# Kernel optimization log

Hardware: AMD Instinct MI355X
Metric: run time of the kernel (lower is better)

Reference implementation:

```python
import jax, jax.numpy as jnp
import numpy as np

INPUT_SIZE = 128
HIDDEN = 256
EPS = 1e-5  # PyTorch BatchNorm1d default


def setup_inputs() -> dict:
    key = jax.random.key(0)
    k1, k2, k3 = jax.random.split(key, 3)
    B, S = 128, 1024
    x = jax.random.normal(k1, (B, S, INPUT_SIZE), dtype=jnp.float32)
    fan_in = INPUT_SIZE + HIDDEN
    bound = 1.0 / np.sqrt(fan_in)
    # Linear(input+hidden -> 4*hidden); stored transposed for x @ W
    W = jax.random.uniform(k2, (fan_in, 4 * HIDDEN), minval=-bound, maxval=bound, dtype=jnp.float32)
    b = jax.random.uniform(k3, (4 * HIDDEN,), minval=-bound, maxval=bound, dtype=jnp.float32)
    gamma = jnp.ones((4, HIDDEN), dtype=jnp.float32)   # per-gate BN weight
    beta = jnp.zeros((4, HIDDEN), dtype=jnp.float32)   # per-gate BN bias
    return {"x": x, "W": W, "b": b, "gamma": gamma, "beta": beta}


def reference(x, W, b, gamma, beta):
    B, S, _ = x.shape
    H = HIDDEN

    def step(carry, x_t):
        hx, cx = carry
        g = jnp.concatenate([x_t, hx], axis=1) @ W + b          # [B, 4H]
        g = g.reshape(B, 4, H)
        # BatchNorm1d (training mode): batch statistics per gate/feature
        mean = g.mean(axis=0)                                   # [4, H]
        var = jnp.mean((g - mean) ** 2, axis=0)                 # biased var
        gn = (g - mean) * jax.lax.rsqrt(var + EPS) * gamma + beta
        i = jax.nn.sigmoid(gn[:, 0])
        f = jax.nn.sigmoid(gn[:, 1])
        c = jnp.tanh(gn[:, 2])
        o = jax.nn.sigmoid(gn[:, 3])
        cy = f * cx + i * c
        hy = o * jnp.tanh(cy)
        return (hy, cy), hy

    h0 = jnp.zeros((B, H), dtype=x.dtype)
    c0 = jnp.zeros((B, H), dtype=x.dtype)
    (hy, cy), outs = jax.lax.scan(step, (h0, c0), jnp.swapaxes(x, 0, 1))
    outputs = jnp.swapaxes(outs, 0, 1)                          # [B, S, H]
    return outputs, hy, cy
```

## Files before the change

kernel.cpp:

```cpp
#include <hip/hip_runtime.h>

#define BATCH 128
#define SEQ   1024
#define INSZ  128
#define HID   256
#define NBLK  32
#define NTHR  512
#define FPB   8
#define EPSV  1e-5f

typedef __attribute__((ext_vector_type(4))) float f32x4;
typedef __attribute__((ext_vector_type(8))) short short8;
typedef __attribute__((ext_vector_type(4))) unsigned u32x4;
typedef unsigned u32;

__device__ __forceinline__ unsigned short f2bf(float f) {
  unsigned u = __builtin_bit_cast(unsigned, f);
  u += 0x7FFFu + ((u >> 16) & 1u);
  return (unsigned short)(u >> 16);
}
__device__ __forceinline__ short8 xcvt(float4 f0, float4 f1) {
  u32 a, b, c, d2;
  asm("v_cvt_pk_bf16_f32 %0, %1, %2" : "=v"(a)  : "v"(f0.x), "v"(f0.y));
  asm("v_cvt_pk_bf16_f32 %0, %1, %2" : "=v"(b)  : "v"(f0.z), "v"(f0.w));
  asm("v_cvt_pk_bf16_f32 %0, %1, %2" : "=v"(c)  : "v"(f1.x), "v"(f1.y));
  asm("v_cvt_pk_bf16_f32 %0, %1, %2" : "=v"(d2) : "v"(f1.z), "v"(f1.w));
  u32x4 t = {a, b, c, d2};
  return __builtin_bit_cast(short8, t);
}

__launch_bounds__(NTHR)
__global__ void bnlstm_kernel(const float* __restrict__ x,
                              const float* __restrict__ W,
                              const float* __restrict__ gamma,
                              const float* __restrict__ beta,
                              float* __restrict__ out,
                              unsigned short* __restrict__ hbuf,
                              u32* __restrict__ flags) {
  __shared__ __attribute__((aligned(16))) unsigned short Zs[32 * 1024];
  __shared__ float red1[2][8][32];
  __shared__ float red2[2][8][32];
  __shared__ float waveTr[8][16][17];
  __shared__ __attribute__((aligned(16))) unsigned short hpack[8][16][8];

  const int tid   = threadIdx.x;
  const int bid   = blockIdx.x;
  const int lane  = tid & 63;
  const int wid   = tid >> 6;
  const int col16 = lane & 15;
  const int kg    = lane >> 4;
  const int d     = col16 & 3;
  const int q     = col16 >> 2;
  const int arow  = wid * 16 + col16;
  const int brow  = wid * 16 + kg * 4 + d;

  short8 wf[2][12];
  for (int cg = 0; cg < 2; ++cg) {
    const int c32 = cg * 16 + col16;
    const int wcol = (c32 & 3) * HID + bid * FPB + (c32 >> 2);
    for (int kt = 0; kt < 12; ++kt) {
      short8 v;
      for (int e = 0; e < 8; ++e)
        v[e] = (short)f2bf(W[(kt * 32 + kg * 8 + e) * 1024 + wcol]);
      wf[cg][kt] = v;
    }
  }
  float gam = 0.f, bet = 0.f;
  if (lane < 32) {
    gam = gamma[(lane & 3) * HID + bid * FPB + (lane >> 2)];
    bet = beta [(lane & 3) * HID + bid * FPB + (lane >> 2)];
  }

  float cst[2] = {0.f, 0.f};
  float hnv[2];

  const float* xbase = x + (size_t)arow * (SEQ * INSZ) + kg * 8;
  float4 xv[8];
  #pragma unroll
  for (int kt = 0; kt < 4; ++kt) {
    xv[2 * kt]     = *(const float4*)(xbase + kt * 32);
    xv[2 * kt + 1] = *(const float4*)(xbase + kt * 32 + 4);
  }

  for (int t = 0; t < SEQ; ++t) {
    const int pR = t & 1;
    f32x4 acc0 = {0.f, 0.f, 0.f, 0.f}, acc1 = {0.f, 0.f, 0.f, 0.f};

    #pragma unroll
    for (int kt = 0; kt < 4; ++kt) {
      short8 ax = xcvt(xv[2 * kt], xv[2 * kt + 1]);
      acc0 = __builtin_amdgcn_mfma_f32_16x16x32_bf16(ax, wf[0][kt], acc0, 0, 0, 0);
      acc1 = __builtin_amdgcn_mfma_f32_16x16x32_bf16(ax, wf[1][kt], acc1, 0, 0, 0);
    }
    if (t + 1 < SEQ) {
      const float* xr = xbase + (size_t)(t + 1) * INSZ;
      #pragma unroll
      for (int kt = 0; kt < 4; ++kt) {
        xv[2 * kt]     = *(const float4*)(xr + kt * 32);
        xv[2 * kt + 1] = *(const float4*)(xr + kt * 32 + 4);
      }
    }

    if (t > 0) {
      {
        const u32 tv = (u32)t;
        while (true) {
          u32 v = (lane < 4)
            ? __hip_atomic_load(&flags[(wid * 4 + lane) * 32], __ATOMIC_RELAXED,
                                __HIP_MEMORY_SCOPE_AGENT)
            : tv;
          if (__all((int)(v >= tv))) break;
          __builtin_amdgcn_s_sleep(1);
        }
      }
      const unsigned short* hsrc = hbuf + pR * (BATCH * HID);
      u32x4 hvv[8];
      #pragma unroll
      for (int k = 0; k < 8; ++k) {
        const int slab = wid * 4 + (k >> 1);
        const int row  = (k & 1) * 64 + lane;
        const unsigned short* ap = hsrc + slab * 1024 + row * 8;
        asm volatile("global_load_dwordx4 %0, %1, off sc0 sc1"
                     : "=v"(hvv[k]) : "v"(ap));
      }
      asm volatile("s_waitcnt vmcnt(0)" ::: "memory");
      __builtin_amdgcn_sched_barrier(0);
      #pragma unroll
      for (int k = 0; k < 8; ++k) {
        const int slab = wid * 4 + (k >> 1);
        const int row  = (k & 1) * 64 + lane;
        *(u32x4*)&Zs[slab * 1024 + row * 8] = hvv[k];
      }
      __syncthreads();

      #pragma unroll
      for (int kt = 0; kt < 8; ++kt) {
        short8 af = *(const short8*)&Zs[(kt * 4 + kg) * 1024 + arow * 8];
        acc0 = __builtin_amdgcn_mfma_f32_16x16x32_bf16(af, wf[0][4 + kt], acc0, 0, 0, 0);
        acc1 = __builtin_amdgcn_mfma_f32_16x16x32_bf16(af, wf[1][4 + kt], acc1, 0, 0, 0);
      }
    }

    {
      float a1 = acc0[0] + acc0[1] + acc0[2] + acc0[3];
      float b1 = acc0[0]*acc0[0] + acc0[1]*acc0[1] + acc0[2]*acc0[2] + acc0[3]*acc0[3];
      float a2 = acc1[0] + acc1[1] + acc1[2] + acc1[3];
      float b2 = acc1[0]*acc1[0] + acc1[1]*acc1[1] + acc1[2]*acc1[2] + acc1[3]*acc1[3];
      a1 += __shfl_xor(a1, 16); b1 += __shfl_xor(b1, 16);
      a1 += __shfl_xor(a1, 32); b1 += __shfl_xor(b1, 32);
      a2 += __shfl_xor(a2, 16); b2 += __shfl_xor(b2, 16);
      a2 += __shfl_xor(a2, 32); b2 += __shfl_xor(b2, 32);
      if (lane < 16) {
        red1[pR][wid][lane] = a1;       red2[pR][wid][lane] = b1;
        red1[pR][wid][16 + lane] = a2;  red2[pR][wid][16 + lane] = b2;
      }
    }
    __syncthreads();

    float sc0v, sh0v, sc1v, sh1v;
    {
      const int cidx = lane & 31;
      float S1 = 0.f, S2 = 0.f;
      #pragma unroll
      for (int w2 = 0; w2 < 8; ++w2) { S1 += red1[pR][w2][cidx]; S2 += red2[pR][w2][cidx]; }
      float mean = S1 * (1.f / BATCH);
      float var  = fmaxf(S2 * (1.f / BATCH) - mean * mean, 0.f);
      float scl = rsqrtf(var + EPSV) * gam;
      float shl = bet - mean * scl;
      sc0v = __shfl(scl, col16);       sh0v = __shfl(shl, col16);
      sc1v = __shfl(scl, 16 + col16);  sh1v = __shfl(shl, 16 + col16);
    }

    #pragma unroll
    for (int cg = 0; cg < 2; ++cg) {
      f32x4 a = cg ? acc1 : acc0;
      const float sc = cg ? sc1v : sc0v, sh = cg ? sh1v : sh0v;
      #pragma unroll
      for (int i = 0; i < 4; ++i)
        waveTr[wid][kg * 4 + i][col16] = a[i] * sc + sh;
      float g0 = waveTr[wid][kg * 4 + d][q * 4 + 0];
      float g1 = waveTr[wid][kg * 4 + d][q * 4 + 1];
      float g2 = waveTr[wid][kg * 4 + d][q * 4 + 2];
      float g3 = waveTr[wid][kg * 4 + d][q * 4 + 3];
      float ig = 1.f / (1.f + __expf(-g0));
      float fg = 1.f / (1.f + __expf(-g1));
      float gg = 1.f - 2.f / (__expf(2.f * g2) + 1.f);
      float og = 1.f / (1.f + __expf(-g3));
      float cn = fg * cst[cg] + ig * gg;
      float hn = og * (1.f - 2.f / (__expf(2.f * cn) + 1.f));
      cst[cg] = cn;
      hnv[cg] = hn;
      hpack[wid][kg * 4 + d][cg * 4 + q] = f2bf(hn);
    }

    if (t < SEQ - 1) {
      if (lane < 16) {
        u32x4 hv = *(const u32x4*)&hpack[wid][lane][0];
        unsigned short* hd = hbuf + (pR ^ 1) * (BATCH * HID)
                           + (bid * 128 + wid * 16 + lane) * 8;
        asm volatile("global_store_dwordx4 %0, %1, off sc0 sc1"
                     :: "v"(hd), "v"(hv) : "memory");
      }
      asm volatile("s_waitcnt vmcnt(0)" ::: "memory");
      __syncthreads();
      if (tid == 0)
        __hip_atomic_store(&flags[bid * 32], (u32)(t + 1),
                           __ATOMIC_RELAXED, __HIP_MEMORY_SCOPE_AGENT);
      float* po = &out[(size_t)brow * (SEQ * HID) + (size_t)t * HID + bid * FPB];
      po[q]     = hnv[0];
      po[4 + q] = hnv[1];
    } else {
      float* po = &out[(size_t)brow * (SEQ * HID) + (size_t)t * HID + bid * FPB];
      po[q]     = hnv[0];
      po[4 + q] = hnv[1];
      float* ph = &out[(size_t)BATCH * SEQ * HID + (size_t)brow * HID + bid * FPB];
      ph[q] = hnv[0];                 ph[4 + q] = hnv[1];
      ph[BATCH * HID + q] = cst[0];   ph[BATCH * HID + 4 + q] = cst[1];
    }
  }
}

extern "C" void kernel_launch(void* const* d_in, const int* in_sizes, int n_in,
                              void* d_out, int out_size, void* d_ws, size_t ws_size,
                              hipStream_t stream) {
  const float* x     = (const float*)d_in[0];
  const float* W     = (const float*)d_in[1];
  const float* gamma = (const float*)d_in[3];
  const float* beta  = (const float*)d_in[4];
  float* out = (float*)d_out;

  u32* flags = (u32*)d_ws;
  unsigned short* hbuf = (unsigned short*)((char*)d_ws + 4096);

  (void)hipMemsetAsync(d_ws, 0, 4096, stream);
  hipLaunchKernelGGL(bnlstm_kernel, dim3(NBLK), dim3(NTHR), 0, stream,
                     x, W, gamma, beta, out, hbuf, flags);
}
```

Measured before the change: 5.278 ms.

## Use per-wave flags and wave-local h loads to drop block barriers

Each wave now publishes its own completion flag, and each consumer wave polls all 32 producer blocks' flags for its own wave index. Each wave loads only the hidden-state rows it needs into its private LDS region, so the two per-step __syncthreads around the h exchange are removed. The sigmoid and tanh divisions are also replaced with hardware reciprocal approximations. This shortens the critical path of the serial recurrence, at the cost of more flag polling traffic and slightly lower precision.

```diff
diff --git a/kernel.cpp b/kernel.cpp
--- a/kernel.cpp
+++ b/kernel.cpp
@@ -105,8 +105,8 @@
       {
         const u32 tv = (u32)t;
         while (true) {
-          u32 v = (lane < 4)
-            ? __hip_atomic_load(&flags[(wid * 4 + lane) * 32], __ATOMIC_RELAXED,
+          u32 v = (lane < NBLK)
+            ? __hip_atomic_load(&flags[(lane * 8 + wid) * 32], __ATOMIC_RELAXED,
                                 __HIP_MEMORY_SCOPE_AGENT)
             : tv;
           if (__all((int)(v >= tv))) break;
@@ -117,25 +117,19 @@
       u32x4 hvv[8];
       #pragma unroll
       for (int k = 0; k < 8; ++k) {
-        const int slab = wid * 4 + (k >> 1);
-        const int row  = (k & 1) * 64 + lane;
-        const unsigned short* ap = hsrc + slab * 1024 + row * 8;
+        const unsigned short* ap = hsrc + ((k * 4 + kg) * 128 + arow) * 8;
         asm volatile("global_load_dwordx4 %0, %1, off sc0 sc1"
                      : "=v"(hvv[k]) : "v"(ap));
       }
       asm volatile("s_waitcnt vmcnt(0)" ::: "memory");
       __builtin_amdgcn_sched_barrier(0);
       #pragma unroll
-      for (int k = 0; k < 8; ++k) {
-        const int slab = wid * 4 + (k >> 1);
-        const int row  = (k & 1) * 64 + lane;
-        *(u32x4*)&Zs[slab * 1024 + row * 8] = hvv[k];
-      }
-      __syncthreads();
+      for (int k = 0; k < 8; ++k)
+        *(u32x4*)&Zs[((k * 4 + kg) * 128 + arow) * 8] = hvv[k];
 
       #pragma unroll
       for (int kt = 0; kt < 8; ++kt) {
-        short8 af = *(const short8*)&Zs[(kt * 4 + kg) * 1024 + arow * 8];
+        short8 af = *(const short8*)&Zs[((kt * 4 + kg) * 128 + arow) * 8];
         acc0 = __builtin_amdgcn_mfma_f32_16x16x32_bf16(af, wf[0][4 + kt], acc0, 0, 0, 0);
         acc1 = __builtin_amdgcn_mfma_f32_16x16x32_bf16(af, wf[1][4 + kt], acc1, 0, 0, 0);
       }
@@ -182,12 +176,12 @@
       float g1 = waveTr[wid][kg * 4 + d][q * 4 + 1];
       float g2 = waveTr[wid][kg * 4 + d][q * 4 + 2];
       float g3 = waveTr[wid][kg * 4 + d][q * 4 + 3];
-      float ig = 1.f / (1.f + __expf(-g0));
-      float fg = 1.f / (1.f + __expf(-g1));
-      float gg = 1.f - 2.f / (__expf(2.f * g2) + 1.f);
-      float og = 1.f / (1.f + __expf(-g3));
+      float ig = __builtin_amdgcn_rcpf(1.f + __expf(-g0));
+      float fg = __builtin_amdgcn_rcpf(1.f + __expf(-g1));
+      float gg = 1.f - 2.f * __builtin_amdgcn_rcpf(__expf(2.f * g2) + 1.f);
+      float og = __builtin_amdgcn_rcpf(1.f + __expf(-g3));
       float cn = fg * cst[cg] + ig * gg;
-      float hn = og * (1.f - 2.f / (__expf(2.f * cn) + 1.f));
+      float hn = og * (1.f - 2.f * __builtin_amdgcn_rcpf(__expf(2.f * cn) + 1.f));
       cst[cg] = cn;
       hnv[cg] = hn;
       hpack[wid][kg * 4 + d][cg * 4 + q] = f2bf(hn);
@@ -202,9 +196,8 @@
                      :: "v"(hd), "v"(hv) : "memory");
       }
       asm volatile("s_waitcnt vmcnt(0)" ::: "memory");
-      __syncthreads();
-      if (tid == 0)
-        __hip_atomic_store(&flags[bid * 32], (u32)(t + 1),
+      if (lane == 0)
+        __hip_atomic_store(&flags[(bid * 8 + wid) * 32], (u32)(t + 1),
                            __ATOMIC_RELAXED, __HIP_MEMORY_SCOPE_AGENT);
       float* po = &out[(size_t)brow * (SEQ * HID) + (size_t)t * HID + bid * FPB];
       po[q]     = hnv[0];
@@ -230,9 +223,9 @@
   float* out = (float*)d_out;
 
   u32* flags = (u32*)d_ws;
-  unsigned short* hbuf = (unsigned short*)((char*)d_ws + 4096);
-
-  (void)hipMemsetAsync(d_ws, 0, 4096, stream);
+  unsigned short* hbuf = (unsigned short*)((char*)d_ws + 32768);
+
+  (void)hipMemsetAsync(d_ws, 0, 32768, stream);
   hipLaunchKernelGGL(bnlstm_kernel, dim3(NBLK), dim3(NTHR), 0, stream,
                      x, W, gamma, beta, out, hbuf, flags);
 }
```

Result: faster. 4.623 ms (-12.4%).
